# Kernel optimization log

Measured on AMD Instinct MI355X. Metric: run time of the kernel, lower is better.

Reference implementation:

```python
import jax, jax.numpy as jnp
import numpy as np

B, S, T = 256, 120, 24   # batch, src frames, predicted frames
D, H = 216, 1024          # input_dim (24 joints x 3x3 rotmat), hidden_dim


def setup_inputs() -> dict:
    key = jax.random.key(0)
    ks = jax.random.split(key, 8)
    s = 0.05  # ~ init_weights uniform(-0.08, 0.08) scale
    return {
        "src": jax.random.normal(ks[0], (B, S, D), jnp.float32),
        "tgt": jax.random.normal(ks[1], (B, T, D), jnp.float32),
        "W_ih": jax.random.normal(ks[2], (4 * H, D), jnp.float32) * s,
        "W_hh": jax.random.normal(ks[3], (4 * H, H), jnp.float32) * s,
        "b_ih": jnp.zeros((4 * H,), jnp.float32),
        "b_hh": jnp.zeros((4 * H,), jnp.float32),
        "W_out": jax.random.normal(ks[4], (D, H), jnp.float32) * s,
        "b_out": jnp.zeros((D,), jnp.float32),
        "max_len": T,
    }


def reference(src, tgt, W_ih, W_hh, b_ih, b_hh, W_out, b_out, max_len):
    # Eval-mode forward: dropout = identity.
    # Encoder: teacher-forced (teacher_forcing_ratio=1.0 -> always feed src[t]).
    def cell(x, h, c):
        # PyTorch LSTM gate order: i, f, g, o
        gates = x @ W_ih.T + b_ih + h @ W_hh.T + b_hh  # [B, 4H]
        i, f, g, o = jnp.split(gates, 4, axis=-1)
        c = jax.nn.sigmoid(f) * c + jax.nn.sigmoid(i) * jnp.tanh(g)
        h = jax.nn.sigmoid(o) * jnp.tanh(c)
        return h, c

    b = src.shape[0]
    h0 = jnp.zeros((b, H), src.dtype)
    c0 = jnp.zeros((b, H), src.dtype)

    # Encoder over src, time-major [S, B, D]
    def enc_step(carry, x):
        h, c = carry
        h, c = cell(x, h, c)
        return (h, c), None

    (h, c), _ = jax.lax.scan(enc_step, (h0, c0), jnp.swapaxes(src, 0, 1))

    # Decoder: first input is last src frame, then feed back projected output
    def dec_step(carry, _):
        h, c, x = carry
        h, c = cell(x, h, c)
        out = h @ W_out.T + b_out  # [B, D]
        return (h, c, out), out

    _, outs = jax.lax.scan(dec_step, (h, c, src[:, -1, :]), None, length=max_len)
    return jnp.swapaxes(outs, 0, 1)  # [B, max_len, D]
```

## Files before the change

### kernel.cpp

```cpp
#include <hip/hip_runtime.h>
#include <hip/hip_bf16.h>

typedef unsigned short u16;
typedef unsigned int   u32;
typedef unsigned long long u64;
typedef __attribute__((ext_vector_type(4)))  float  f32x4;
typedef __attribute__((ext_vector_type(8)))  short  short8;
typedef __attribute__((ext_vector_type(16))) float  f32x16;

#define MB     256
#define SRCT   120
#define DECT   24
#define NSTEP  144
#define DIN    216
#define HDIM   1024
#define KXP    224
#define KA     1248
#define NGATE  4096
#define OUTD   216
#define NWG    256

#define OFF_SRCBF 0u
#define OFF_H     13762560u
#define OFF_XDEC  14811136u
#define OFF_WCAT  14925824u
#define OFF_WO    25149440u
#define OFF_BAR   25591808u

__device__ __forceinline__ u16 f2bf(float f) {
    union { float f; unsigned v; } c; c.f = f;
    return (u16)((c.v + 0x7FFFu + ((c.v >> 16) & 1u)) >> 16);
}
__device__ __forceinline__ float sigm(float x)  { return 1.0f / (1.0f + __expf(-x)); }
__device__ __forceinline__ float tanh_(float x) { return 1.0f - 2.0f / (1.0f + __expf(2.0f * x)); }

__device__ __forceinline__ void astore(u64* p, u64 v) {
    __hip_atomic_store(p, v, __ATOMIC_RELAXED, __HIP_MEMORY_SCOPE_AGENT);
}

template <int AUX>
__device__ __forceinline__ void dma16(const u16* g, u16* l) {
    __builtin_amdgcn_global_load_lds(
        (const __attribute__((address_space(1))) void*)g,
        (__attribute__((address_space(3))) void*)l, 16, 0, AUX);
}

__device__ __forceinline__ void bar_arrive(u32* gslots, int s, u32 gen) {
    __syncthreads();
    if (threadIdx.x == 0)
        __hip_atomic_store(gslots + s, gen, __ATOMIC_RELAXED, __HIP_MEMORY_SCOPE_AGENT);
}
__device__ __forceinline__ void bar_wait(u32* gslots, u32 gen) {
    if (threadIdx.x < 64) {
        const int idx = threadIdx.x & 31;
        while (__hip_atomic_load(gslots + idx, __ATOMIC_RELAXED, __HIP_MEMORY_SCOPE_AGENT) < gen)
            __builtin_amdgcn_s_sleep(1);
    }
    __syncthreads();
}

__global__ void prep_kernel(const float* __restrict__ src,
                            const float* __restrict__ W_ih,
                            const float* __restrict__ W_hh,
                            const float* __restrict__ W_out,
                            u16* __restrict__ srcbf, u16* __restrict__ H,
                            u16* __restrict__ Xd,    u16* __restrict__ Wcat,
                            u16* __restrict__ Wo,    u32* __restrict__ bar) {
    const int nS  = SRCT * 8 * 28 * 256;
    const int nW  = NGATE * KA;
    const int nWo = OUTD * HDIM;
    const int nH  = MB * HDIM;
    const int nXd = 8 * 28 * 256;
    const int nB  = 8 * 64;
    const int total = nS + nW + nWo + nH + nXd + nB;
    for (int i = blockIdx.x * blockDim.x + threadIdx.x; i < total; i += gridDim.x * blockDim.x) {
        if (i < nS) {
            int r = i & 255, i2 = i >> 8;
            int m = r >> 3, e = r & 7;
            int oct = i2 % 28, q = i2 / 28;
            int gi = q & 7, t = q >> 3;
            int col = oct * 8 + e, b = gi * 32 + m;
            srcbf[i] = (col < DIN) ? f2bf(src[((size_t)b * SRCT + t) * DIN + col]) : (u16)0;
        } else if (i < nS + nW) {
            int j = i - nS;
            int r = j / KA, col = j % KA;
            u16 v = 0;
            if (col < DIN)       v = f2bf(W_ih[(size_t)r * DIN + col]);
            else if (col >= KXP) v = f2bf(W_hh[(size_t)r * HDIM + (col - KXP)]);
            Wcat[j] = v;
        } else if (i < nS + nW + nWo) {
            int j = i - nS - nW;
            Wo[j] = f2bf(W_out[j]);
        } else if (i < nS + nW + nWo + nH) {
            H[i - nS - nW - nWo] = 0;
        } else if (i < nS + nW + nWo + nH + nXd) {
            Xd[i - nS - nW - nWo - nH] = 0;
        } else {
            bar[i - nS - nW - nWo - nH - nXd] = 0;
        }
    }
}

__global__ void __launch_bounds__(256, 1)
lstm_persist(const u16* __restrict__ srcbf, u16* __restrict__ H,
             u16* __restrict__ Xd, const u16* __restrict__ Wcat,
             const u16* __restrict__ Wo,
             const float* __restrict__ b_ih, const float* __restrict__ b_hh,
             const float* __restrict__ b_out,
             float* __restrict__ dout, u32* __restrict__ bar)
{
    __shared__ __align__(16) u16  Ach[156 * 32 * 8];
    __shared__ __align__(16) float G2[16 * 32 * 36];
    __shared__ __align__(16) u16  Hx[4 * 32 * 8];

    const int bid  = blockIdx.x;
    const int g    = bid & 7;
    const int s    = bid >> 3;
    const int b0   = g * 32;
    const int tid  = threadIdx.x;
    const int p    = tid >> 6;
    const int lane = tid & 63;
    const int l31  = lane & 31;
    const int kg   = lane >> 5;

    u32* gslots = bar + g * 64;
    const u16* Xdg = Xd + (size_t)g * 7168;

    const int ktb = p * 20 - (p == 3 ? 1 : 0);
    const int ktc = (p < 2) ? 20 : 19;

    short8 Bfrag[4][20];
#pragma unroll
    for (int gg = 0; gg < 4; ++gg) {
        const u16* pw = Wcat + (size_t)(gg * 1024 + s * 32 + l31) * KA + kg * 8;
#pragma unroll
        for (int j = 0; j < 20; ++j) {
            int kt = ktb + j; if (kt > 77) kt = 77;
            Bfrag[gg][j] = *(const short8*)(pw + kt * 16);
        }
    }

    const int cs = tid & 31;
    const int bq = tid >> 5;
    float creg[4] = {0.f, 0.f, 0.f, 0.f};
    const int hcg = s * 32 + cs;
    const float bI  = b_ih[hcg]        + b_hh[hcg];
    const float bF  = b_ih[1024 + hcg] + b_hh[1024 + hcg];
    const float bG_ = b_ih[2048 + hcg] + b_hh[2048 + hcg];
    const float bO  = b_ih[3072 + hcg] + b_hh[3072 + hcg];
    const float bOutv = (s < 7 && hcg < OUTD) ? b_out[hcg] : 0.f;

    u32 gen = 0;

    {
        const u16* xsb0 = srcbf + (size_t)g * 7168;
#pragma unroll
        for (int j = 0; j < 4; ++j) {
            int idx = p + 4 * j;
            if (idx < 14) dma16<0>(xsb0 + idx * 512 + lane * 8, Ach + idx * 512);
        }
        const u16* h0 = H + (size_t)g * 32768;
#pragma unroll
        for (int j = 0; j < 16; ++j) {
            int idx = p * 16 + j;
            dma16<17>(h0 + idx * 512 + lane * 8, Ach + 7168 + idx * 512);
        }
    }
    __syncthreads();

    for (int t = 0; t < NSTEP; ++t) {
        u16* HTn = H + (size_t)((t + 1) & 1) * (MB * HDIM);
        const u16* hnext = HTn + (size_t)g * 32768;

        f32x16 acc[4] = {f32x16{}, f32x16{}, f32x16{}, f32x16{}};
#pragma unroll
        for (int j = 0; j < 20; ++j) {
            if (j < ktc) {
                const int oct = 2 * (ktb + j) + kg;
                short8 af = *(const short8*)(Ach + (size_t)(oct * 32 + l31) * 8);
                acc[0] = __builtin_amdgcn_mfma_f32_32x32x16_bf16(af, Bfrag[0][j], acc[0], 0, 0, 0);
                acc[1] = __builtin_amdgcn_mfma_f32_32x32x16_bf16(af, Bfrag[1][j], acc[1], 0, 0, 0);
                acc[2] = __builtin_amdgcn_mfma_f32_32x32x16_bf16(af, Bfrag[2][j], acc[2], 0, 0, 0);
                acc[3] = __builtin_amdgcn_mfma_f32_32x32x16_bf16(af, Bfrag[3][j], acc[3], 0, 0, 0);
            }
        }
#pragma unroll
        for (int gg = 0; gg < 4; ++gg) {
#pragma unroll
            for (int rq = 0; rq < 4; ++rq) {
                f32x4 v;
                v[0] = acc[gg][rq * 4 + 0]; v[1] = acc[gg][rq * 4 + 1];
                v[2] = acc[gg][rq * 4 + 2]; v[3] = acc[gg][rq * 4 + 3];
                *(f32x4*)&G2[(size_t)((gg * 4 + p) * 32 + l31) * 36 + rq * 8 + kg * 4] = v;
            }
        }
        __syncthreads();

        {
            f32x4 sg[4];
#pragma unroll
            for (int gg = 0; gg < 4; ++gg) {
                f32x4 a = *(const f32x4*)&G2[(size_t)((gg * 4 + 0) * 32 + cs) * 36 + bq * 4];
#pragma unroll
                for (int pp = 1; pp < 4; ++pp)
                    a += *(const f32x4*)&G2[(size_t)((gg * 4 + pp) * 32 + cs) * 36 + bq * 4];
                sg[gg] = a;
            }
#pragma unroll
            for (int i = 0; i < 4; ++i) {
                float gi = sg[0][i] + bI, gf = sg[1][i] + bF;
                float gG = sg[2][i] + bG_, go = sg[3][i] + bO;
                float c = sigm(gf) * creg[i] + sigm(gi) * tanh_(gG);
                creg[i] = c;
                Hx[(cs >> 3) * 256 + (bq * 4 + i) * 8 + (cs & 7)] = f2bf(sigm(go) * tanh_(c));
            }
        }
        __syncthreads();
        astore((u64*)HTn + (size_t)g * 8192 + s * 256 + tid, ((const u64*)Hx)[tid]);

        if (t < SRCT) {
            bar_arrive(gslots, s, ++gen);
            int tt2 = (t + 1 < SRCT) ? (t + 1) : (SRCT - 1);
            const u16* xsb2 = srcbf + (size_t)(tt2 * 8 + g) * 7168 / 8 * 8;
            xsb2 = srcbf + (size_t)(tt2 * 8 + g) * 28 * 256;
#pragma unroll
            for (int j = 0; j < 4; ++j) {
                int idx = p + 4 * j;
                if (idx < 14) dma16<0>(xsb2 + idx * 512 + lane * 8, Ach + idx * 512);
            }
            bar_wait(gslots, gen);
#pragma unroll
            for (int j = 0; j < 16; ++j) {
                int idx = p * 16 + j;
                dma16<17>(hnext + idx * 512 + lane * 8, Ach + 7168 + idx * 512);
            }
            __syncthreads();
        } else {
            const int d = t - SRCT;
            bar_arrive(gslots, s, ++gen);
            bar_wait(gslots, gen);
#pragma unroll
            for (int j = 0; j < 16; ++j) {
                int idx = p * 16 + j;
                dma16<17>(hnext + idx * 512 + lane * 8, Ach + 7168 + idx * 512);
            }
            __syncthreads();
            if (s < 7) {
                f32x16 oacc = {};
                const int orow = (s * 32 + l31 < OUTD) ? (s * 32 + l31) : (OUTD - 1);
                const u16* wob = Wo + (size_t)orow * HDIM + kg * 8;
#pragma unroll
                for (int j = 0; j < 16; ++j) {
                    int kt = p * 16 + j;
                    short8 af = *(const short8*)(Ach + (size_t)((28 + 2 * kt + kg) * 32 + l31) * 8);
                    short8 bf = *(const short8*)(wob + (size_t)kt * 16);
                    oacc = __builtin_amdgcn_mfma_f32_32x32x16_bf16(af, bf, oacc, 0, 0, 0);
                }
#pragma unroll
                for (int rq = 0; rq < 4; ++rq) {
                    f32x4 v;
                    v[0] = oacc[rq * 4 + 0]; v[1] = oacc[rq * 4 + 1];
                    v[2] = oacc[rq * 4 + 2]; v[3] = oacc[rq * 4 + 3];
                    *(f32x4*)&G2[(size_t)(p * 32 + l31) * 36 + rq * 8 + kg * 4] = v;
                }
            }
            __syncthreads();
            if (s < 7) {
                const int  ocol = s * 32 + cs;
                const bool real = ocol < OUTD;
                f32x4 S = *(const f32x4*)&G2[(size_t)(0 * 32 + cs) * 36 + bq * 4];
#pragma unroll
                for (int pp = 1; pp < 4; ++pp)
                    S += *(const f32x4*)&G2[(size_t)(pp * 32 + cs) * 36 + bq * 4];
#pragma unroll
                for (int i = 0; i < 4; ++i) {
                    float v = real ? (S[i] + bOutv) : 0.f;
                    Hx[(cs >> 3) * 256 + (bq * 4 + i) * 8 + (cs & 7)] = real ? f2bf(v) : (u16)0;
                    if (real)
                        dout[(size_t)(b0 + bq * 4 + i) * (DECT * OUTD) + (size_t)d * OUTD + ocol] = v;
                }
            }
            __syncthreads();
            if (s < 7)
                astore((u64*)Xdg + s * 256 + tid, ((const u64*)Hx)[tid]);
            if (t < NSTEP - 1) {
                bar_arrive(gslots, s, ++gen);
                bar_wait(gslots, gen);
#pragma unroll
                for (int j = 0; j < 4; ++j) {
                    int idx = p + 4 * j;
                    if (idx < 14) dma16<17>(Xdg + idx * 512 + lane * 8, Ach + idx * 512);
                }
                __syncthreads();
            }
        }
    }
}

extern "C" void kernel_launch(void* const* d_in, const int* in_sizes, int n_in,
                              void* d_out, int out_size, void* d_ws, size_t ws_size,
                              hipStream_t stream) {
    const float* src   = (const float*)d_in[0];
    const float* W_ih  = (const float*)d_in[2];
    const float* W_hh  = (const float*)d_in[3];
    const float* b_ih  = (const float*)d_in[4];
    const float* b_hh  = (const float*)d_in[5];
    const float* W_out = (const float*)d_in[6];
    const float* b_out = (const float*)d_in[7];
    float* out = (float*)d_out;

    char* ws = (char*)d_ws;
    u16* srcbf = (u16*)(ws + OFF_SRCBF);
    u16* H     = (u16*)(ws + OFF_H);
    u16* Xd    = (u16*)(ws + OFF_XDEC);
    u16* Wcat  = (u16*)(ws + OFF_WCAT);
    u16* Wo    = (u16*)(ws + OFF_WO);
    u32* bar   = (u32*)(ws + OFF_BAR);

    hipLaunchKernelGGL(prep_kernel, dim3(2048), dim3(256), 0, stream,
                       src, W_ih, W_hh, W_out, srcbf, H, Xd, Wcat, Wo, bar);

    hipLaunchKernelGGL(lstm_persist, dim3(NWG), dim3(256), 0, stream,
                       srcbf, H, Xd, Wcat, Wo, b_ih, b_hh, b_out, out, bar);
}
```

Measured before the change: 948.4 us.

## Stream A operands directly from global memory and switch to counter-based barriers

The LDS staging buffer for the activation/hidden operands is removed. Each wave now loads its A fragments straight from global memory with cache-bypassing (sc0 sc1) loads, keeping an 8-deep software prefetch in registers that is interleaved with the MFMAs. The grid barrier changes from per-slot generation stores polled by 32 lanes to one atomic fetch-add counter per step polled by a single thread. The aim is to drop the bulk LDS copy and the extra syncthreads after each barrier, and to cut barrier polling traffic. In exchange every wave repeats global or L2 loads on the critical path, and register pressure rises.

Measured after the change: 868.9 us. 8.4% less time.

```diff
diff --git a/kernel.cpp b/kernel.cpp
--- a/kernel.cpp
+++ b/kernel.cpp
@@ -38,22 +38,26 @@
     __hip_atomic_store(p, v, __ATOMIC_RELAXED, __HIP_MEMORY_SCOPE_AGENT);
 }
 
-template <int AUX>
-__device__ __forceinline__ void dma16(const u16* g, u16* l) {
-    __builtin_amdgcn_global_load_lds(
-        (const __attribute__((address_space(1))) void*)g,
-        (__attribute__((address_space(3))) void*)l, 16, 0, AUX);
-}
-
-__device__ __forceinline__ void bar_arrive(u32* gslots, int s, u32 gen) {
+__device__ __forceinline__ short8 ld_sc(const u16* p) {
+    short8 r;
+    asm volatile("global_load_dwordx4 %0, %1, off sc0 sc1" : "=v"(r) : "v"(p));
+    return r;
+}
+template <int N>
+__device__ __forceinline__ void vwait() {
+    asm volatile("s_waitcnt vmcnt(%0)" :: "n"(N));
+    __builtin_amdgcn_sched_barrier(0);
+}
+
+__device__ __forceinline__ void g_arrive(u32* slots, int k) {
     __syncthreads();
     if (threadIdx.x == 0)
-        __hip_atomic_store(gslots + s, gen, __ATOMIC_RELAXED, __HIP_MEMORY_SCOPE_AGENT);
-}
-__device__ __forceinline__ void bar_wait(u32* gslots, u32 gen) {
-    if (threadIdx.x < 64) {
-        const int idx = threadIdx.x & 31;
-        while (__hip_atomic_load(gslots + idx, __ATOMIC_RELAXED, __HIP_MEMORY_SCOPE_AGENT) < gen)
+        __hip_atomic_fetch_add(slots + (k & 63), 1u, __ATOMIC_RELAXED, __HIP_MEMORY_SCOPE_AGENT);
+}
+__device__ __forceinline__ void g_wait(u32* slots, int k) {
+    if (threadIdx.x == 0) {
+        const u32 tgt = 32u * (u32)((k >> 6) + 1);
+        while (__hip_atomic_load(slots + (k & 63), __ATOMIC_RELAXED, __HIP_MEMORY_SCOPE_AGENT) < tgt)
             __builtin_amdgcn_s_sleep(1);
     }
     __syncthreads();
@@ -101,6 +105,53 @@
     }
 }
 
+template <int J>
+__device__ __forceinline__ void gate_issue(short8 (&av)[20], const u16* xb, const u16* hb,
+                                           int ktb, int lo) {
+    int kt = ktb + J;
+    if (kt > 77) kt = 77;
+    const int o2 = 2 * kt;
+    const u16* base = (o2 < 28) ? (xb + o2 * 256) : (hb + (o2 - 28) * 256);
+    av[J] = ld_sc(base + lo);
+}
+template <int J>
+__device__ __forceinline__ void gate_pro(short8 (&av)[20], const u16* xb, const u16* hb,
+                                         int ktb, int lo) {
+    gate_issue<J>(av, xb, hb, ktb, lo);
+    if constexpr (J + 1 < 8) gate_pro<J + 1>(av, xb, hb, ktb, lo);
+}
+template <int J>
+__device__ __forceinline__ void gate_body(short8 (&av)[20], short8 (&Bf)[4][20], f32x16 (&acc)[4],
+                                          const u16* xb, const u16* hb, int ktb, int lo) {
+    if constexpr (J + 8 < 20) gate_issue<J + 8>(av, xb, hb, ktb, lo);
+    vwait<(J + 8 < 20) ? 8 : (19 - J)>();
+    acc[0] = __builtin_amdgcn_mfma_f32_32x32x16_bf16(av[J], Bf[0][J], acc[0], 0, 0, 0);
+    acc[1] = __builtin_amdgcn_mfma_f32_32x32x16_bf16(av[J], Bf[1][J], acc[1], 0, 0, 0);
+    acc[2] = __builtin_amdgcn_mfma_f32_32x32x16_bf16(av[J], Bf[2][J], acc[2], 0, 0, 0);
+    acc[3] = __builtin_amdgcn_mfma_f32_32x32x16_bf16(av[J], Bf[3][J], acc[3], 0, 0, 0);
+    if constexpr (J + 1 < 20) gate_body<J + 1>(av, Bf, acc, xb, hb, ktb, lo);
+}
+
+template <int J>
+__device__ __forceinline__ void out_issue(short8 (&av)[16], const u16* hb, int kt0, int lo) {
+    const int o2 = 2 * (kt0 + J);
+    av[J] = ld_sc(hb + o2 * 256 + lo);
+}
+template <int J>
+__device__ __forceinline__ void out_pro(short8 (&av)[16], const u16* hb, int kt0, int lo) {
+    out_issue<J>(av, hb, kt0, lo);
+    if constexpr (J + 1 < 8) out_pro<J + 1>(av, hb, kt0, lo);
+}
+template <int J>
+__device__ __forceinline__ void out_body(short8 (&av)[16], f32x16& oacc, const u16* hb,
+                                         const u16* wob, int kt0, int lo) {
+    if constexpr (J + 8 < 16) out_issue<J + 8>(av, hb, kt0, lo);
+    vwait<(J + 8 < 16) ? 8 : (15 - J)>();
+    short8 bf = *(const short8*)(wob + (size_t)(kt0 + J) * 16);
+    oacc = __builtin_amdgcn_mfma_f32_32x32x16_bf16(av[J], bf, oacc, 0, 0, 0);
+    if constexpr (J + 1 < 16) out_body<J + 1>(av, oacc, hb, wob, kt0, lo);
+}
+
 __global__ void __launch_bounds__(256, 1)
 lstm_persist(const u16* __restrict__ srcbf, u16* __restrict__ H,
              u16* __restrict__ Xd, const u16* __restrict__ Wcat,
@@ -109,9 +160,9 @@
              const float* __restrict__ b_out,
              float* __restrict__ dout, u32* __restrict__ bar)
 {
-    __shared__ __align__(16) u16  Ach[156 * 32 * 8];
     __shared__ __align__(16) float G2[16 * 32 * 36];
     __shared__ __align__(16) u16  Hx[4 * 32 * 8];
+    __shared__ __align__(16) char lds_pad[8192];
 
     const int bid  = blockIdx.x;
     const int g    = bid & 7;
@@ -122,9 +173,12 @@
     const int lane = tid & 63;
     const int l31  = lane & 31;
     const int kg   = lane >> 5;
+    const int lo   = kg * 256 + l31 * 8;
+
+    if (tid == 255) *(volatile char*)lds_pad = 0;
 
     u32* gslots = bar + g * 64;
-    const u16* Xdg = Xd + (size_t)g * 7168;
+    u16* Xdg = Xd + (size_t)g * 7168;
 
     const int ktb = p * 20 - (p == 3 ? 1 : 0);
     const int ktc = (p < 2) ? 20 : 19;
@@ -135,8 +189,12 @@
         const u16* pw = Wcat + (size_t)(gg * 1024 + s * 32 + l31) * KA + kg * 8;
 #pragma unroll
         for (int j = 0; j < 20; ++j) {
-            int kt = ktb + j; if (kt > 77) kt = 77;
-            Bfrag[gg][j] = *(const short8*)(pw + kt * 16);
+            if (j < ktc) {
+                int kt = ktb + j;
+                Bfrag[gg][j] = *(const short8*)(pw + (size_t)kt * 16);
+            } else {
+                Bfrag[gg][j] = short8{};
+            }
         }
     }
 
@@ -150,39 +208,20 @@
     const float bO  = b_ih[3072 + hcg] + b_hh[3072 + hcg];
     const float bOutv = (s < 7 && hcg < OUTD) ? b_out[hcg] : 0.f;
 
-    u32 gen = 0;
-
-    {
-        const u16* xsb0 = srcbf + (size_t)g * 7168;
-#pragma unroll
-        for (int j = 0; j < 4; ++j) {
-            int idx = p + 4 * j;
-            if (idx < 14) dma16<0>(xsb0 + idx * 512 + lane * 8, Ach + idx * 512);
-        }
-        const u16* h0 = H + (size_t)g * 32768;
-#pragma unroll
-        for (int j = 0; j < 16; ++j) {
-            int idx = p * 16 + j;
-            dma16<17>(h0 + idx * 512 + lane * 8, Ach + 7168 + idx * 512);
-        }
-    }
-    __syncthreads();
-
     for (int t = 0; t < NSTEP; ++t) {
-        u16* HTn = H + (size_t)((t + 1) & 1) * (MB * HDIM);
+        const u16* hb    = H + (size_t)(t & 1) * (MB * HDIM) + (size_t)g * 32768;
+        u16*       HTn   = H + (size_t)((t + 1) & 1) * (MB * HDIM);
         const u16* hnext = HTn + (size_t)g * 32768;
+        const u16* xb;
+        if (t < SRCT)       xb = srcbf + (size_t)(t * 8 + g) * 7168;
+        else if (t == SRCT) xb = srcbf + (size_t)((SRCT - 1) * 8 + g) * 7168;
+        else                xb = Xdg;
 
         f32x16 acc[4] = {f32x16{}, f32x16{}, f32x16{}, f32x16{}};
-#pragma unroll
-        for (int j = 0; j < 20; ++j) {
-            if (j < ktc) {
-                const int oct = 2 * (ktb + j) + kg;
-                short8 af = *(const short8*)(Ach + (size_t)(oct * 32 + l31) * 8);
-                acc[0] = __builtin_amdgcn_mfma_f32_32x32x16_bf16(af, Bfrag[0][j], acc[0], 0, 0, 0);
-                acc[1] = __builtin_amdgcn_mfma_f32_32x32x16_bf16(af, Bfrag[1][j], acc[1], 0, 0, 0);
-                acc[2] = __builtin_amdgcn_mfma_f32_32x32x16_bf16(af, Bfrag[2][j], acc[2], 0, 0, 0);
-                acc[3] = __builtin_amdgcn_mfma_f32_32x32x16_bf16(af, Bfrag[3][j], acc[3], 0, 0, 0);
-            }
+        {
+            short8 av[20];
+            gate_pro<0>(av, xb, hb, ktb, lo);
+            gate_body<0>(av, Bfrag, acc, xb, hb, ktb, lo);
         }
 #pragma unroll
         for (int gg = 0; gg < 4; ++gg) {
@@ -219,43 +258,20 @@
         astore((u64*)HTn + (size_t)g * 8192 + s * 256 + tid, ((const u64*)Hx)[tid]);
 
         if (t < SRCT) {
-            bar_arrive(gslots, s, ++gen);
-            int tt2 = (t + 1 < SRCT) ? (t + 1) : (SRCT - 1);
-            const u16* xsb2 = srcbf + (size_t)(tt2 * 8 + g) * 7168 / 8 * 8;
-            xsb2 = srcbf + (size_t)(tt2 * 8 + g) * 28 * 256;
-#pragma unroll
-            for (int j = 0; j < 4; ++j) {
-                int idx = p + 4 * j;
-                if (idx < 14) dma16<0>(xsb2 + idx * 512 + lane * 8, Ach + idx * 512);
-            }
-            bar_wait(gslots, gen);
-#pragma unroll
-            for (int j = 0; j < 16; ++j) {
-                int idx = p * 16 + j;
-                dma16<17>(hnext + idx * 512 + lane * 8, Ach + 7168 + idx * 512);
-            }
-            __syncthreads();
+            g_arrive(gslots, t);
+            g_wait(gslots, t);
         } else {
-            const int d = t - SRCT;
-            bar_arrive(gslots, s, ++gen);
-            bar_wait(gslots, gen);
-#pragma unroll
-            for (int j = 0; j < 16; ++j) {
-                int idx = p * 16 + j;
-                dma16<17>(hnext + idx * 512 + lane * 8, Ach + 7168 + idx * 512);
-            }
-            __syncthreads();
+            const int d  = t - SRCT;
+            const int k1 = SRCT + 2 * d;
+            g_arrive(gslots, k1);
+            g_wait(gslots, k1);
             if (s < 7) {
                 f32x16 oacc = {};
                 const int orow = (s * 32 + l31 < OUTD) ? (s * 32 + l31) : (OUTD - 1);
                 const u16* wob = Wo + (size_t)orow * HDIM + kg * 8;
-#pragma unroll
-                for (int j = 0; j < 16; ++j) {
-                    int kt = p * 16 + j;
-                    short8 af = *(const short8*)(Ach + (size_t)((28 + 2 * kt + kg) * 32 + l31) * 8);
-                    short8 bf = *(const short8*)(wob + (size_t)kt * 16);
-                    oacc = __builtin_amdgcn_mfma_f32_32x32x16_bf16(af, bf, oacc, 0, 0, 0);
-                }
+                short8 av2[16];
+                out_pro<0>(av2, hnext, p * 16, lo);
+                out_body<0>(av2, oacc, hnext, wob, p * 16, lo);
 #pragma unroll
                 for (int rq = 0; rq < 4; ++rq) {
                     f32x4 v;
@@ -284,14 +300,8 @@
             if (s < 7)
                 astore((u64*)Xdg + s * 256 + tid, ((const u64*)Hx)[tid]);
             if (t < NSTEP - 1) {
-                bar_arrive(gslots, s, ++gen);
-                bar_wait(gslots, gen);
-#pragma unroll
-                for (int j = 0; j < 4; ++j) {
-                    int idx = p + 4 * j;
-                    if (idx < 14) dma16<17>(Xdg + idx * 512 + lane * 8, Ach + idx * 512);
-                }
-                __syncthreads();
+                g_arrive(gslots, k1 + 1);
+                g_wait(gslots, k1 + 1);
             }
         }
     }
```
